# Performance work log

Measured on AMD Instinct MI355X. Metric: run time of the kernel, lower is better.

## Reference

```python
import jax, jax.numpy as jnp
import numpy as np

D_MODEL = 1024
HEAD_DIM = D_MODEL // 16  # num_heads=16, used only for the softmax scale
EPS = 1e-5


def _layernorm(x, g, b):
    mu = jnp.mean(x, axis=-1, keepdims=True)
    var = jnp.var(x, axis=-1, keepdims=True)
    return (x - mu) * jax.lax.rsqrt(var + EPS) * g + b


def setup_inputs() -> dict:
    key = jax.random.key(0)
    ks = jax.random.split(key, 16)
    d, dff = D_MODEL, 4 * D_MODEL
    s = 1.0 / np.sqrt(d)
    inp = {
        "x": jax.random.normal(ks[0], (4, 2048, d), dtype=jnp.float32),
        "wq": jax.random.normal(ks[1], (d, d), dtype=jnp.float32) * s,
        "bq": jnp.zeros((d,), jnp.float32),
        "wk": jax.random.normal(ks[2], (d, d), dtype=jnp.float32) * s,
        "bk": jnp.zeros((d,), jnp.float32),
        "wv": jax.random.normal(ks[3], (d, d), dtype=jnp.float32) * s,
        "bv": jnp.zeros((d,), jnp.float32),
        "wo": jax.random.normal(ks[4], (d, d), dtype=jnp.float32) * s,
        "bo": jnp.zeros((d,), jnp.float32),
        "w1": jax.random.normal(ks[5], (d, dff), dtype=jnp.float32) * s,
        "b1": jnp.zeros((dff,), jnp.float32),
        "w2": jax.random.normal(ks[6], (dff, d), dtype=jnp.float32) * (1.0 / np.sqrt(dff)),
        "b2": jnp.zeros((d,), jnp.float32),
        "g1": jnp.ones((d,), jnp.float32),
        "be1": jnp.zeros((d,), jnp.float32),
        "g2": jnp.ones((d,), jnp.float32),
        "be2": jnp.zeros((d,), jnp.float32),
    }
    return inp


def reference(x, wq, bq, wk, bk, wv, bv, wo, bo, w1, b1, w2, b2, g1, be1, g2, be2):
    # --- attention sub-block (NOTE: no head split in original module) ---
    residual = x
    h = _layernorm(x, g1, be1)
    q = h @ wq + bq
    k = h @ wk + bk
    v = h @ wv + bv
    scale = 1.0 / np.sqrt(HEAD_DIM)
    scores = jnp.einsum("bsd,btd->bst", q, k) * scale  # [B,S,S]
    attn = jax.nn.softmax(scores, axis=-1)
    ctx = jnp.einsum("bst,btd->bsd", attn, v)
    x = ctx @ wo + bo + residual
    # --- MLP sub-block ---
    residual = x
    h = _layernorm(x, g2, be2)
    h = jax.nn.gelu(h @ w1 + b1, approximate=False)
    return h @ w2 + b2 + residual
```

## Files before the change

kernel.cpp:

```cpp
#include <hip/hip_runtime.h>
#include <hip/hip_bf16.h>

typedef __hip_bfloat16 bf16;
typedef __attribute__((ext_vector_type(8))) short short8;
typedef __attribute__((ext_vector_type(4))) float floatx4;

__device__ __forceinline__ unsigned short f2bf(float x) {
  unsigned u = __builtin_bit_cast(unsigned, x);
  unsigned r = (u + 0x7fffu + ((u >> 16) & 1u)) >> 16;
  return (unsigned short)r;
}

#define GLL(g, l) __builtin_amdgcn_global_load_lds(                                  \
    (const __attribute__((address_space(1))) void*)(g),                              \
    (__attribute__((address_space(3))) void*)(l), 16, 0, 0)

template <int N> __device__ __forceinline__ void vmwait() {
  asm volatile("s_waitcnt vmcnt(%0)" ::"i"(N) : "memory");
}

__global__ __launch_bounds__(256) void wtrans_kernel(const float* __restrict__ in,
                                                     bf16* __restrict__ out,
                                                     int K, int N) {
  __shared__ float tile[32][33];
  int tx = threadIdx.x, ty = threadIdx.y;
  int n0 = blockIdx.x * 32, k0 = blockIdx.y * 32;
#pragma unroll
  for (int i = 0; i < 32; i += 8)
    tile[ty + i][tx] = in[(size_t)(k0 + ty + i) * N + (n0 + tx)];
  __syncthreads();
#pragma unroll
  for (int i = 0; i < 32; i += 8)
    out[(size_t)(n0 + ty + i) * K + (k0 + tx)] = __float2bfloat16(tile[tx][ty + i]);
}

__global__ __launch_bounds__(256) void ln_kernel(const float* __restrict__ x,
                                                 const float* __restrict__ g,
                                                 const float* __restrict__ b,
                                                 bf16* __restrict__ out) {
  const int D = 1024;
  size_t row = blockIdx.x;
  int t = threadIdx.x;
  float4 v = ((const float4*)(x + row * D))[t];
  float s  = v.x + v.y + v.z + v.w;
  float ss = v.x * v.x + v.y * v.y + v.z * v.z + v.w * v.w;
#pragma unroll
  for (int off = 32; off > 0; off >>= 1) {
    s  += __shfl_xor(s, off);
    ss += __shfl_xor(ss, off);
  }
  __shared__ float rs[4], rss[4];
  int wv = t >> 6;
  if ((t & 63) == 0) { rs[wv] = s; rss[wv] = ss; }
  __syncthreads();
  s  = rs[0] + rs[1] + rs[2] + rs[3];
  ss = rss[0] + rss[1] + rss[2] + rss[3];
  float mu  = s * (1.f / D);
  float inv = rsqrtf(ss * (1.f / D) - mu * mu + 1e-5f);
  float4 gv = ((const float4*)g)[t];
  float4 bv = ((const float4*)b)[t];
  ushort4 o;
  o.x = f2bf((v.x - mu) * inv * gv.x + bv.x);
  o.y = f2bf((v.y - mu) * inv * gv.y + bv.y);
  o.z = f2bf((v.z - mu) * inv * gv.z + bv.z);
  o.w = f2bf((v.w - mu) * inv * gv.w + bv.w);
  ((ushort4*)(out + row * D))[t] = o;
}

__global__ __launch_bounds__(256) void softmax_kernel(float* sc) {
  const int S = 2048;
  float* p = sc + (size_t)blockIdx.x * S;
  int t = threadIdx.x;
  float4 v0 = ((const float4*)p)[2 * t];
  float4 v1 = ((const float4*)p)[2 * t + 1];
  float f[8] = {v0.x, v0.y, v0.z, v0.w, v1.x, v1.y, v1.z, v1.w};
  float m = f[0];
#pragma unroll
  for (int j = 1; j < 8; ++j) m = fmaxf(m, f[j]);
#pragma unroll
  for (int off = 32; off > 0; off >>= 1) m = fmaxf(m, __shfl_xor(m, off));
  __shared__ float r1[4], r2[4];
  int wv = t >> 6;
  if ((t & 63) == 0) r1[wv] = m;
  __syncthreads();
  m = fmaxf(fmaxf(r1[0], r1[1]), fmaxf(r1[2], r1[3]));
  float s = 0.f;
#pragma unroll
  for (int j = 0; j < 8; ++j) { f[j] = __expf(f[j] - m); s += f[j]; }
#pragma unroll
  for (int off = 32; off > 0; off >>= 1) s += __shfl_xor(s, off);
  if ((t & 63) == 0) r2[wv] = s;
  __syncthreads();
  s = r2[0] + r2[1] + r2[2] + r2[3];
  float inv = 1.f / s;
  unsigned u0 = f2bf(f[0] * inv), u1 = f2bf(f[1] * inv);
  unsigned u2 = f2bf(f[2] * inv), u3 = f2bf(f[3] * inv);
  unsigned u4 = f2bf(f[4] * inv), u5 = f2bf(f[5] * inv);
  unsigned u6 = f2bf(f[6] * inv), u7 = f2bf(f[7] * inv);
  uint4 o;
  o.x = u0 | (u1 << 16);
  o.y = u2 | (u3 << 16);
  o.z = u4 | (u5 << 16);
  o.w = u6 | (u7 << 16);
  ((uint4*)p)[t] = o;
}

template <int NF, bool OUT_BF16, bool HAS_BIAS, bool HAS_RES, bool GELU, bool VTR>
__global__ __launch_bounds__(512, 2) void gemm4q(
    const bf16* __restrict__ A, int lda, size_t sA,
    const bf16* __restrict__ BT, int ldb, size_t sB,
    void* Cv, size_t sC,
    const float* __restrict__ bias, const float* res, bf16* vtr,
    int N, int K, float alpha, int gx, int gy) {
  constexpr int BN = NF * 64;
  constexpr int NI = NF / 2;
  constexpr int BHALF = NF == 4 ? 16384 : 8192;
  constexpr int W_A = 4;
  constexpr int W_B = NF == 4 ? 4 : 3;
  __shared__ __align__(16) char lds[65536 + (NF == 4 ? 65536 : 32768)];
  char* const ldsA = lds;
  char* const ldsB = lds + 65536;

  const int tid = threadIdx.x;
  const int lane = tid & 63;
  const int wave = tid >> 6;
  const int wm = wave >> 2, wn = wave & 3;
  const int lr = lane & 15, lq = lane >> 4;

  int id = blockIdx.x;
  const int nwg = gridDim.x;
  if ((nwg & 7) == 0) id = (id & 7) * (nwg >> 3) + (id >> 3);
  const int bx = id % gx;
  const int rem = id / gx;
  const int by = rem % gy;
  const int bz = rem / gy;
  const int m0 = by * 256, n0 = bx * BN;

  const int srow = tid >> 3;
  const int schunk = ((tid & 7) ^ (srow & 7)) * 8;
  const bf16* gA = A + sA * bz + (size_t)(m0 + srow) * lda + schunk;
  const bf16* gB = BT + sB * bz + (size_t)(n0 + srow) * ldb + schunk;

  const int nk = K >> 6;

  auto stA = [&](int tt, int h) {
    if (tt < nk) {
      const bf16* s = gA + (size_t)(h * 128) * lda + (size_t)tt * 64;
      char* d = ldsA + (((tt & 1) * 2 + h) << 14) + tid * 16;
      GLL(s, d);
      GLL(s + (size_t)64 * lda, d + 8192);
    }
  };
  auto stB = [&](int tt, int h) {
    if (tt < nk) {
      const bf16* s = gB + (size_t)(h * (BN / 2)) * ldb + (size_t)tt * 64;
      char* d = ldsB + ((tt & 1) * 2 + h) * BHALF + tid * 16;
      GLL(s, d);
      if constexpr (NF == 4) GLL(s + (size_t)64 * ldb, d + 8192);
    }
  };

  const int aB0 = (wm * 64 + lr) * 128 + ((lq ^ (lr & 7)) << 4);
  const int aB1 = aB0 ^ 64;
  const int bRow = (NF == 4) ? (wn * 32 + lr) : (wn * 16 + lr);
  const int bB0 = bRow * 128 + ((lq ^ (lr & 7)) << 4);
  const int bB1 = bB0 ^ 64;

  floatx4 acc[2][2][4][NI] = {};

  stA(0, 0); stB(0, 0); stB(0, 1); stA(0, 1);
  vmwait<W_B>();
  __builtin_amdgcn_s_barrier();

  for (int t = 0; t < nk; ++t) {
    const char* As0 = ldsA + (((t & 1) * 2 + 0) << 14);
    const char* As1 = ldsA + (((t & 1) * 2 + 1) << 14);
    const char* Bs0 = ldsB + ((t & 1) * 2 + 0) * BHALF;
    const char* Bs1 = ldsB + ((t & 1) * 2 + 1) * BHALF;
    short8 a0[4], a1[4], b0[NI], b1[NI];

#pragma unroll
    for (int mi = 0; mi < 4; ++mi) {
      a0[mi] = *(const short8*)(As0 + aB0 + mi * 2048);
      a1[mi] = *(const short8*)(As0 + aB1 + mi * 2048);
    }
#pragma unroll
    for (int ni = 0; ni < NI; ++ni) {
      b0[ni] = *(const short8*)(Bs0 + bB0 + ni * 2048);
      b1[ni] = *(const short8*)(Bs0 + bB1 + ni * 2048);
    }
    stA(t + 1, 0);
    asm volatile("s_waitcnt lgkmcnt(0)" ::: "memory");
    __builtin_amdgcn_sched_barrier(0);
    __builtin_amdgcn_s_setprio(1);
#pragma unroll
    for (int mi = 0; mi < 4; ++mi)
#pragma unroll
      for (int ni = 0; ni < NI; ++ni)
        acc[0][0][mi][ni] = __builtin_amdgcn_mfma_f32_16x16x32_bf16(a0[mi], b0[ni], acc[0][0][mi][ni], 0, 0, 0);
#pragma unroll
    for (int mi = 0; mi < 4; ++mi)
#pragma unroll
      for (int ni = 0; ni < NI; ++ni)
        acc[0][0][mi][ni] = __builtin_amdgcn_mfma_f32_16x16x32_bf16(a1[mi], b1[ni], acc[0][0][mi][ni], 0, 0, 0);
    __builtin_amdgcn_s_setprio(0);
    vmwait<W_A>();
    __builtin_amdgcn_s_barrier();

#pragma unroll
    for (int ni = 0; ni < NI; ++ni) {
      b0[ni] = *(const short8*)(Bs1 + bB0 + ni * 2048);
      b1[ni] = *(const short8*)(Bs1 + bB1 + ni * 2048);
    }
    stB(t + 1, 0);
    asm volatile("s_waitcnt lgkmcnt(0)" ::: "memory");
    __builtin_amdgcn_sched_barrier(0);
    __builtin_amdgcn_s_setprio(1);
#pragma unroll
    for (int mi = 0; mi < 4; ++mi)
#pragma unroll
      for (int ni = 0; ni < NI; ++ni)
        acc[0][1][mi][ni] = __builtin_amdgcn_mfma_f32_16x16x32_bf16(a0[mi], b0[ni], acc[0][1][mi][ni], 0, 0, 0);
#pragma unroll
    for (int mi = 0; mi < 4; ++mi)
#pragma unroll
      for (int ni = 0; ni < NI; ++ni)
        acc[0][1][mi][ni] = __builtin_amdgcn_mfma_f32_16x16x32_bf16(a1[mi], b1[ni], acc[0][1][mi][ni], 0, 0, 0);
    __builtin_amdgcn_s_setprio(0);
    vmwait<W_B>();
    __builtin_amdgcn_s_barrier();

#pragma unroll
    for (int mi = 0; mi < 4; ++mi) {
      a0[mi] = *(const short8*)(As1 + aB0 + mi * 2048);
      a1[mi] = *(const short8*)(As1 + aB1 + mi * 2048);
    }
    stB(t + 1, 1);
    asm volatile("s_waitcnt lgkmcnt(0)" ::: "memory");
    __builtin_amdgcn_sched_barrier(0);
    __builtin_amdgcn_s_setprio(1);
#pragma unroll
    for (int mi = 0; mi < 4; ++mi)
#pragma unroll
      for (int ni = 0; ni < NI; ++ni)
        acc[1][1][mi][ni] = __builtin_amdgcn_mfma_f32_16x16x32_bf16(a0[mi], b0[ni], acc[1][1][mi][ni], 0, 0, 0);
#pragma unroll
    for (int mi = 0; mi < 4; ++mi)
#pragma unroll
      for (int ni = 0; ni < NI; ++ni)
        acc[1][1][mi][ni] = __builtin_amdgcn_mfma_f32_16x16x32_bf16(a1[mi], b1[ni], acc[1][1][mi][ni], 0, 0, 0);
    __builtin_amdgcn_s_setprio(0);
    __builtin_amdgcn_s_barrier();

#pragma unroll
    for (int ni = 0; ni < NI; ++ni) {
      b0[ni] = *(const short8*)(Bs0 + bB0 + ni * 2048);
      b1[ni] = *(const short8*)(Bs0 + bB1 + ni * 2048);
    }
    stA(t + 1, 1);
    asm volatile("s_waitcnt lgkmcnt(0)" ::: "memory");
    __builtin_amdgcn_sched_barrier(0);
    __builtin_amdgcn_s_setprio(1);
#pragma unroll
    for (int mi = 0; mi < 4; ++mi)
#pragma unroll
      for (int ni = 0; ni < NI; ++ni)
        acc[1][0][mi][ni] = __builtin_amdgcn_mfma_f32_16x16x32_bf16(a0[mi], b0[ni], acc[1][0][mi][ni], 0, 0, 0);
#pragma unroll
    for (int mi = 0; mi < 4; ++mi)
#pragma unroll
      for (int ni = 0; ni < NI; ++ni)
        acc[1][0][mi][ni] = __builtin_amdgcn_mfma_f32_16x16x32_bf16(a1[mi], b1[ni], acc[1][0][mi][ni], 0, 0, 0);
    __builtin_amdgcn_s_setprio(0);
    vmwait<W_B>();
    __builtin_amdgcn_s_barrier();
  }

  float* Cf = (float*)Cv;
  bf16* Cb = (bf16*)Cv;
  const size_t cb = sC * bz;
#pragma unroll
  for (int mq = 0; mq < 2; ++mq)
#pragma unroll
    for (int nq = 0; nq < 2; ++nq)
#pragma unroll
      for (int mi = 0; mi < 4; ++mi) {
        const int row = m0 + mq * 128 + wm * 64 + mi * 16 + lq * 4;
#pragma unroll
        for (int ni = 0; ni < NI; ++ni) {
          const int col = n0 + nq * (BN / 2) + wn * (BN / 8) + ni * 16 + lr;
          const float bb = HAS_BIAS ? bias[col] : 0.f;
#pragma unroll
          for (int r = 0; r < 4; ++r) {
            float val = acc[mq][nq][mi][ni][r] * alpha + bb;
            if (GELU) val = 0.5f * val * (1.f + erff(val * 0.70710678118654752f));
            if (HAS_RES) val += res[(size_t)(row + r) * N + col];
            const size_t idx = cb + (size_t)(row + r) * N + col;
            if (OUT_BF16) Cb[idx] = __float2bfloat16(val);
            else Cf[idx] = val;
            if (VTR) {
              if (col >= 2048) {
                const int rr = row + r;
                vtr[(((size_t)(rr >> 11) << 10) + (col - 2048)) * 2048 + (rr & 2047)] =
                    __float2bfloat16(val);
              }
            }
          }
        }
      }
}

extern "C" void kernel_launch(void* const* d_in, const int* in_sizes, int n_in,
                              void* d_out, int out_size, void* d_ws, size_t ws_size,
                              hipStream_t stream) {
  const int B = 4, S = 2048, D = 1024, DFF = 4096;
  const int M = B * S;
  const float* x   = (const float*)d_in[0];
  const float* wq  = (const float*)d_in[1];
  const float* bq  = (const float*)d_in[2];
  const float* wk  = (const float*)d_in[3];
  const float* bk  = (const float*)d_in[4];
  const float* wv  = (const float*)d_in[5];
  const float* bv  = (const float*)d_in[6];
  const float* wo  = (const float*)d_in[7];
  const float* bo  = (const float*)d_in[8];
  const float* w1  = (const float*)d_in[9];
  const float* b1  = (const float*)d_in[10];
  const float* w2  = (const float*)d_in[11];
  const float* b2  = (const float*)d_in[12];
  const float* g1  = (const float*)d_in[13];
  const float* be1 = (const float*)d_in[14];
  const float* g2  = (const float*)d_in[15];
  const float* be2 = (const float*)d_in[16];
  float* out = (float*)d_out;

  char* wsb = (char*)d_ws;
  const size_t MB1 = 1ull << 20;
  bf16* wqkvT = (bf16*)(wsb + 0 * MB1);
  bf16* woT   = (bf16*)(wsb + 6 * MB1);
  bf16* w1T   = (bf16*)(wsb + 8 * MB1);
  bf16* w2T   = (bf16*)(wsb + 16 * MB1);
  float* bqkv = (float*)(wsb + 24 * MB1);
  bf16* h     = (bf16*)(wsb + 25 * MB1);
  bf16* qkv   = (bf16*)(wsb + 41 * MB1);
  bf16* hidden = (bf16*)(wsb + 41 * MB1);
  bf16* vTall = (bf16*)(wsb + 89 * MB1);
  float* sc   = (float*)(wsb + 105 * MB1);

  int chunk = 1;
  if (ws_size > 105 * MB1) {
    size_t c = (ws_size - 105 * MB1) / (16 * MB1);
    chunk = (int)(c > 4 ? 4 : (c < 1 ? 1 : c));
  }

  dim3 tb(32, 8);
  wtrans_kernel<<<dim3(32, 32), tb, 0, stream>>>(wq, wqkvT, D, D);
  wtrans_kernel<<<dim3(32, 32), tb, 0, stream>>>(wk, wqkvT + (size_t)1024 * 1024, D, D);
  wtrans_kernel<<<dim3(32, 32), tb, 0, stream>>>(wv, wqkvT + (size_t)2048 * 1024, D, D);
  wtrans_kernel<<<dim3(32, 32), tb, 0, stream>>>(wo, woT, D, D);
  wtrans_kernel<<<dim3(128, 32), tb, 0, stream>>>(w1, w1T, D, DFF);
  wtrans_kernel<<<dim3(32, 128), tb, 0, stream>>>(w2, w2T, DFF, D);
  hipMemcpyAsync(bqkv, bq, 4096, hipMemcpyDeviceToDevice, stream);
  hipMemcpyAsync(bqkv + 1024, bk, 4096, hipMemcpyDeviceToDevice, stream);
  hipMemcpyAsync(bqkv + 2048, bv, 4096, hipMemcpyDeviceToDevice, stream);

  ln_kernel<<<M, 256, 0, stream>>>(x, g1, be1, h);

  gemm4q<2, true, true, false, false, true><<<24 * 32, 512, 0, stream>>>(
      h, D, 0, wqkvT, D, 0, qkv, 0, bqkv, nullptr, vTall, 3072, D, 1.f, 24, 32);

  for (int b0 = 0; b0 < B; b0 += chunk) {
    int c = (B - b0 < chunk) ? (B - b0) : chunk;
    gemm4q<4, false, false, false, false, false><<<64 * c, 512, 0, stream>>>(
        qkv + (size_t)b0 * S * 3072, 3072, (size_t)S * 3072,
        qkv + (size_t)b0 * S * 3072 + 1024, 3072, (size_t)S * 3072,
        sc, (size_t)S * S, nullptr, nullptr, nullptr, S, D, 0.125f, 8, 8);
    softmax_kernel<<<c * S, 256, 0, stream>>>(sc);
    gemm4q<2, true, false, false, false, false><<<64 * c, 512, 0, stream>>>(
        (const bf16*)sc, 2 * S, (size_t)S * 2 * S,
        vTall + (size_t)b0 * D * S, S, (size_t)D * S,
        h + (size_t)b0 * S * D, (size_t)S * D, nullptr, nullptr, nullptr, D, S, 1.f, 8, 8);
  }

  gemm4q<2, false, true, true, false, false><<<8 * 32, 512, 0, stream>>>(
      h, D, 0, woT, D, 0, out, 0, bo, x, nullptr, D, D, 1.f, 8, 32);

  ln_kernel<<<M, 256, 0, stream>>>(out, g2, be2, h);

  gemm4q<4, true, true, false, true, false><<<16 * 32, 512, 0, stream>>>(
      h, D, 0, w1T, D, 0, hidden, 0, b1, nullptr, nullptr, DFF, D, 1.f, 16, 32);

  gemm4q<2, false, true, true, false, false><<<8 * 32, 512, 0, stream>>>(
      hidden, DFF, 0, w2T, DFF, 0, out, 0, b2, out, nullptr, D, DFF, 1.f, 8, 32);
}
```

Baseline: 473.4 us.

## Peel last K-iteration and use inline ds_read with immediate offsets in GEMM

Rewrites the GEMM main loop to peel the final K tile into an epilogue. This removes the per-load bounds checks on the global-to-LDS prefetch, and the peeled tile drains outstanding loads with exact vmcnt waits. LDS fragment reads become inline-asm ds_read_b128 with immediate offsets from a 32-bit LDS base, which cuts address arithmetic. The fourth quarter-step now reuses A fragments from the third step, with B in separate registers and one fewer barrier per iteration. The hand-counted waitcnt values and the larger code size add risk of ordering bugs or register pressure.

```diff
diff --git a/kernel.cpp b/kernel.cpp
--- a/kernel.cpp
+++ b/kernel.cpp
@@ -4,6 +4,7 @@
 typedef __hip_bfloat16 bf16;
 typedef __attribute__((ext_vector_type(8))) short short8;
 typedef __attribute__((ext_vector_type(4))) float floatx4;
+typedef __attribute__((address_space(3))) char c3;
 
 __device__ __forceinline__ unsigned short f2bf(float x) {
   unsigned u = __builtin_bit_cast(unsigned, x);
@@ -17,6 +18,15 @@
 
 template <int N> __device__ __forceinline__ void vmwait() {
   asm volatile("s_waitcnt vmcnt(%0)" ::"i"(N) : "memory");
+}
+template <int OFF> __device__ __forceinline__ short8 dsr(unsigned a) {
+  short8 r;
+  asm volatile("ds_read_b128 %0, %1 offset:%2" : "=v"(r) : "v"(a), "i"(OFF));
+  return r;
+}
+__device__ __forceinline__ void lgkm0_fence() {
+  asm volatile("s_waitcnt lgkmcnt(0)" ::: "memory");
+  __builtin_amdgcn_sched_barrier(0);
 }
 
 __global__ __launch_bounds__(256) void wtrans_kernel(const float* __restrict__ in,
@@ -106,7 +116,7 @@
 }
 
 template <int NF, bool OUT_BF16, bool HAS_BIAS, bool HAS_RES, bool GELU, bool VTR>
-__global__ __launch_bounds__(512, 2) void gemm4q(
+__global__ __launch_bounds__(512, 2) void gemm6(
     const bf16* __restrict__ A, int lda, size_t sA,
     const bf16* __restrict__ BT, int ldb, size_t sB,
     void* Cv, size_t sC,
@@ -115,11 +125,11 @@
   constexpr int BN = NF * 64;
   constexpr int NI = NF / 2;
   constexpr int BHALF = NF == 4 ? 16384 : 8192;
-  constexpr int W_A = 4;
-  constexpr int W_B = NF == 4 ? 4 : 3;
-  __shared__ __align__(16) char lds[65536 + (NF == 4 ? 65536 : 32768)];
-  char* const ldsA = lds;
-  char* const ldsB = lds + 65536;
+  constexpr int LB = NF == 4 ? 2 : 1;
+  constexpr int W_AB = 2 + LB;
+  __shared__ __align__(16) char lds_storage[65536 + (NF == 4 ? 65536 : 32768)];
+  const unsigned ldsAu = (unsigned)(uintptr_t)(c3*)lds_storage;
+  const unsigned ldsBu = ldsAu + 65536;
 
   const int tid = threadIdx.x;
   const int lane = tid & 63;
@@ -144,54 +154,45 @@
   const int nk = K >> 6;
 
   auto stA = [&](int tt, int h) {
-    if (tt < nk) {
-      const bf16* s = gA + (size_t)(h * 128) * lda + (size_t)tt * 64;
-      char* d = ldsA + (((tt & 1) * 2 + h) << 14) + tid * 16;
-      GLL(s, d);
-      GLL(s + (size_t)64 * lda, d + 8192);
-    }
+    const bf16* s = gA + (size_t)(h * 128) * lda + (size_t)tt * 64;
+    char* d = lds_storage + (((tt & 1) * 2 + h) << 14) + tid * 16;
+    GLL(s, d);
+    GLL(s + (size_t)64 * lda, d + 8192);
   };
   auto stB = [&](int tt, int h) {
-    if (tt < nk) {
-      const bf16* s = gB + (size_t)(h * (BN / 2)) * ldb + (size_t)tt * 64;
-      char* d = ldsB + ((tt & 1) * 2 + h) * BHALF + tid * 16;
-      GLL(s, d);
-      if constexpr (NF == 4) GLL(s + (size_t)64 * ldb, d + 8192);
-    }
+    const bf16* s = gB + (size_t)(h * (BN / 2)) * ldb + (size_t)tt * 64;
+    char* d = lds_storage + 65536 + ((tt & 1) * 2 + h) * BHALF + tid * 16;
+    GLL(s, d);
+    if constexpr (NF == 4) GLL(s + (size_t)64 * ldb, d + 8192);
   };
 
-  const int aB0 = (wm * 64 + lr) * 128 + ((lq ^ (lr & 7)) << 4);
-  const int aB1 = aB0 ^ 64;
-  const int bRow = (NF == 4) ? (wn * 32 + lr) : (wn * 16 + lr);
-  const int bB0 = bRow * 128 + ((lq ^ (lr & 7)) << 4);
-  const int bB1 = bB0 ^ 64;
+  const unsigned aB0 = (wm * 64 + lr) * 128 + ((lq ^ (lr & 7)) << 4);
+  const unsigned bRow = (NF == 4) ? (wn * 32 + lr) : (wn * 16 + lr);
+  const unsigned bB0 = bRow * 128 + ((lq ^ (lr & 7)) << 4);
 
   floatx4 acc[2][2][4][NI] = {};
 
   stA(0, 0); stB(0, 0); stB(0, 1); stA(0, 1);
-  vmwait<W_B>();
+  vmwait<W_AB>();
   __builtin_amdgcn_s_barrier();
 
-  for (int t = 0; t < nk; ++t) {
-    const char* As0 = ldsA + (((t & 1) * 2 + 0) << 14);
-    const char* As1 = ldsA + (((t & 1) * 2 + 1) << 14);
-    const char* Bs0 = ldsB + ((t & 1) * 2 + 0) * BHALF;
-    const char* Bs1 = ldsB + ((t & 1) * 2 + 1) * BHALF;
-    short8 a0[4], a1[4], b0[NI], b1[NI];
-
-#pragma unroll
-    for (int mi = 0; mi < 4; ++mi) {
-      a0[mi] = *(const short8*)(As0 + aB0 + mi * 2048);
-      a1[mi] = *(const short8*)(As0 + aB1 + mi * 2048);
-    }
-#pragma unroll
-    for (int ni = 0; ni < NI; ++ni) {
-      b0[ni] = *(const short8*)(Bs0 + bB0 + ni * 2048);
-      b1[ni] = *(const short8*)(Bs0 + bB1 + ni * 2048);
-    }
+  for (int t = 0; t + 1 < nk; ++t) {
+    const unsigned As0 = ldsAu + (((t & 1) * 2 + 0) << 14);
+    const unsigned As1 = As0 + 16384;
+    const unsigned Bs0 = ldsBu + ((t & 1) * 2 + 0) * BHALF;
+    const unsigned Bs1 = Bs0 + BHALF;
+    short8 a0[4], a1[4], b0[NI], b1[NI], c0[NI], c1[NI];
+
     stA(t + 1, 0);
-    asm volatile("s_waitcnt lgkmcnt(0)" ::: "memory");
-    __builtin_amdgcn_sched_barrier(0);
+    {
+      const unsigned aA = As0 + aB0, aX = aA ^ 64;
+      a0[0] = dsr<0>(aA);  a0[1] = dsr<2048>(aA);  a0[2] = dsr<4096>(aA);  a0[3] = dsr<6144>(aA);
+      a1[0] = dsr<0>(aX);  a1[1] = dsr<2048>(aX);  a1[2] = dsr<4096>(aX);  a1[3] = dsr<6144>(aX);
+      const unsigned bA = Bs0 + bB0, bX = bA ^ 64;
+      b0[0] = dsr<0>(bA); b1[0] = dsr<0>(bX);
+      if constexpr (NI > 1) { b0[1] = dsr<2048>(bA); b1[1] = dsr<2048>(bX); }
+    }
+    lgkm0_fence();
     __builtin_amdgcn_s_setprio(1);
 #pragma unroll
     for (int mi = 0; mi < 4; ++mi)
@@ -204,17 +205,16 @@
       for (int ni = 0; ni < NI; ++ni)
         acc[0][0][mi][ni] = __builtin_amdgcn_mfma_f32_16x16x32_bf16(a1[mi], b1[ni], acc[0][0][mi][ni], 0, 0, 0);
     __builtin_amdgcn_s_setprio(0);
-    vmwait<W_A>();
+    vmwait<4>();
     __builtin_amdgcn_s_barrier();
 
-#pragma unroll
-    for (int ni = 0; ni < NI; ++ni) {
-      b0[ni] = *(const short8*)(Bs1 + bB0 + ni * 2048);
-      b1[ni] = *(const short8*)(Bs1 + bB1 + ni * 2048);
-    }
     stB(t + 1, 0);
-    asm volatile("s_waitcnt lgkmcnt(0)" ::: "memory");
-    __builtin_amdgcn_sched_barrier(0);
+    {
+      const unsigned bA = Bs1 + bB0, bX = bA ^ 64;
+      b0[0] = dsr<0>(bA); b1[0] = dsr<0>(bX);
+      if constexpr (NI > 1) { b0[1] = dsr<2048>(bA); b1[1] = dsr<2048>(bX); }
+    }
+    lgkm0_fence();
     __builtin_amdgcn_s_setprio(1);
 #pragma unroll
     for (int mi = 0; mi < 4; ++mi)
@@ -227,17 +227,16 @@
       for (int ni = 0; ni < NI; ++ni)
         acc[0][1][mi][ni] = __builtin_amdgcn_mfma_f32_16x16x32_bf16(a1[mi], b1[ni], acc[0][1][mi][ni], 0, 0, 0);
     __builtin_amdgcn_s_setprio(0);
-    vmwait<W_B>();
+    vmwait<W_AB>();
     __builtin_amdgcn_s_barrier();
 
-#pragma unroll
-    for (int mi = 0; mi < 4; ++mi) {
-      a0[mi] = *(const short8*)(As1 + aB0 + mi * 2048);
-      a1[mi] = *(const short8*)(As1 + aB1 + mi * 2048);
-    }
     stB(t + 1, 1);
-    asm volatile("s_waitcnt lgkmcnt(0)" ::: "memory");
-    __builtin_amdgcn_sched_barrier(0);
+    {
+      const unsigned aA = As1 + aB0, aX = aA ^ 64;
+      a0[0] = dsr<0>(aA);  a0[1] = dsr<2048>(aA);  a0[2] = dsr<4096>(aA);  a0[3] = dsr<6144>(aA);
+      a1[0] = dsr<0>(aX);  a1[1] = dsr<2048>(aX);  a1[2] = dsr<4096>(aX);  a1[3] = dsr<6144>(aX);
+    }
+    lgkm0_fence();
     __builtin_amdgcn_s_setprio(1);
 #pragma unroll
     for (int mi = 0; mi < 4; ++mi)
@@ -250,30 +249,110 @@
       for (int ni = 0; ni < NI; ++ni)
         acc[1][1][mi][ni] = __builtin_amdgcn_mfma_f32_16x16x32_bf16(a1[mi], b1[ni], acc[1][1][mi][ni], 0, 0, 0);
     __builtin_amdgcn_s_setprio(0);
+    stA(t + 1, 1);
+    {
+      const unsigned bA = Bs0 + bB0, bX = bA ^ 64;
+      c0[0] = dsr<0>(bA); c1[0] = dsr<0>(bX);
+      if constexpr (NI > 1) { c0[1] = dsr<2048>(bA); c1[1] = dsr<2048>(bX); }
+    }
+    lgkm0_fence();
+    __builtin_amdgcn_s_setprio(1);
+#pragma unroll
+    for (int mi = 0; mi < 4; ++mi)
+#pragma unroll
+      for (int ni = 0; ni < NI; ++ni)
+        acc[1][0][mi][ni] = __builtin_amdgcn_mfma_f32_16x16x32_bf16(a0[mi], c0[ni], acc[1][0][mi][ni], 0, 0, 0);
+#pragma unroll
+    for (int mi = 0; mi < 4; ++mi)
+#pragma unroll
+      for (int ni = 0; ni < NI; ++ni)
+        acc[1][0][mi][ni] = __builtin_amdgcn_mfma_f32_16x16x32_bf16(a1[mi], c1[ni], acc[1][0][mi][ni], 0, 0, 0);
+    __builtin_amdgcn_s_setprio(0);
+    vmwait<W_AB>();
     __builtin_amdgcn_s_barrier();
-
-#pragma unroll
-    for (int ni = 0; ni < NI; ++ni) {
-      b0[ni] = *(const short8*)(Bs0 + bB0 + ni * 2048);
-      b1[ni] = *(const short8*)(Bs0 + bB1 + ni * 2048);
-    }
-    stA(t + 1, 1);
-    asm volatile("s_waitcnt lgkmcnt(0)" ::: "memory");
-    __builtin_amdgcn_sched_barrier(0);
-    __builtin_amdgcn_s_setprio(1);
-#pragma unroll
-    for (int mi = 0; mi < 4; ++mi)
-#pragma unroll
-      for (int ni = 0; ni < NI; ++ni)
-        acc[1][0][mi][ni] = __builtin_amdgcn_mfma_f32_16x16x32_bf16(a0[mi], b0[ni], acc[1][0][mi][ni], 0, 0, 0);
-#pragma unroll
-    for (int mi = 0; mi < 4; ++mi)
-#pragma unroll
-      for (int ni = 0; ni < NI; ++ni)
-        acc[1][0][mi][ni] = __builtin_amdgcn_mfma_f32_16x16x32_bf16(a1[mi], b1[ni], acc[1][0][mi][ni], 0, 0, 0);
-    __builtin_amdgcn_s_setprio(0);
-    vmwait<W_B>();
+  }
+
+  {
+    const int t = nk - 1;
+    const unsigned As0 = ldsAu + (((t & 1) * 2 + 0) << 14);
+    const unsigned As1 = As0 + 16384;
+    const unsigned Bs0 = ldsBu + ((t & 1) * 2 + 0) * BHALF;
+    const unsigned Bs1 = Bs0 + BHALF;
+    short8 a0[4], a1[4], b0[NI], b1[NI], c0[NI], c1[NI];
+
+    {
+      const unsigned aA = As0 + aB0, aX = aA ^ 64;
+      a0[0] = dsr<0>(aA);  a0[1] = dsr<2048>(aA);  a0[2] = dsr<4096>(aA);  a0[3] = dsr<6144>(aA);
+      a1[0] = dsr<0>(aX);  a1[1] = dsr<2048>(aX);  a1[2] = dsr<4096>(aX);  a1[3] = dsr<6144>(aX);
+      const unsigned bA = Bs0 + bB0, bX = bA ^ 64;
+      b0[0] = dsr<0>(bA); b1[0] = dsr<0>(bX);
+      if constexpr (NI > 1) { b0[1] = dsr<2048>(bA); b1[1] = dsr<2048>(bX); }
+    }
+    lgkm0_fence();
+#pragma unroll
+    for (int mi = 0; mi < 4; ++mi)
+#pragma unroll
+      for (int ni = 0; ni < NI; ++ni)
+        acc[0][0][mi][ni] = __builtin_amdgcn_mfma_f32_16x16x32_bf16(a0[mi], b0[ni], acc[0][0][mi][ni], 0, 0, 0);
+#pragma unroll
+    for (int mi = 0; mi < 4; ++mi)
+#pragma unroll
+      for (int ni = 0; ni < NI; ++ni)
+        acc[0][0][mi][ni] = __builtin_amdgcn_mfma_f32_16x16x32_bf16(a1[mi], b1[ni], acc[0][0][mi][ni], 0, 0, 0);
+    vmwait<2>();
     __builtin_amdgcn_s_barrier();
+
+    {
+      const unsigned bA = Bs1 + bB0, bX = bA ^ 64;
+      b0[0] = dsr<0>(bA); b1[0] = dsr<0>(bX);
+      if constexpr (NI > 1) { b0[1] = dsr<2048>(bA); b1[1] = dsr<2048>(bX); }
+    }
+    lgkm0_fence();
+#pragma unroll
+    for (int mi = 0; mi < 4; ++mi)
+#pragma unroll
+      for (int ni = 0; ni < NI; ++ni)
+        acc[0][1][mi][ni] = __builtin_amdgcn_mfma_f32_16x16x32_bf16(a0[mi], b0[ni], acc[0][1][mi][ni], 0, 0, 0);
+#pragma unroll
+    for (int mi = 0; mi < 4; ++mi)
+#pragma unroll
+      for (int ni = 0; ni < NI; ++ni)
+        acc[0][1][mi][ni] = __builtin_amdgcn_mfma_f32_16x16x32_bf16(a1[mi], b1[ni], acc[0][1][mi][ni], 0, 0, 0);
+    vmwait<0>();
+    __builtin_amdgcn_s_barrier();
+
+    {
+      const unsigned aA = As1 + aB0, aX = aA ^ 64;
+      a0[0] = dsr<0>(aA);  a0[1] = dsr<2048>(aA);  a0[2] = dsr<4096>(aA);  a0[3] = dsr<6144>(aA);
+      a1[0] = dsr<0>(aX);  a1[1] = dsr<2048>(aX);  a1[2] = dsr<4096>(aX);  a1[3] = dsr<6144>(aX);
+    }
+    lgkm0_fence();
+#pragma unroll
+    for (int mi = 0; mi < 4; ++mi)
+#pragma unroll
+      for (int ni = 0; ni < NI; ++ni)
+        acc[1][1][mi][ni] = __builtin_amdgcn_mfma_f32_16x16x32_bf16(a0[mi], b0[ni], acc[1][1][mi][ni], 0, 0, 0);
+#pragma unroll
+    for (int mi = 0; mi < 4; ++mi)
+#pragma unroll
+      for (int ni = 0; ni < NI; ++ni)
+        acc[1][1][mi][ni] = __builtin_amdgcn_mfma_f32_16x16x32_bf16(a1[mi], b1[ni], acc[1][1][mi][ni], 0, 0, 0);
+    {
+      const unsigned bA = Bs0 + bB0, bX = bA ^ 64;
+      c0[0] = dsr<0>(bA); c1[0] = dsr<0>(bX);
+      if constexpr (NI > 1) { c0[1] = dsr<2048>(bA); c1[1] = dsr<2048>(bX); }
+    }
+    lgkm0_fence();
+#pragma unroll
+    for (int mi = 0; mi < 4; ++mi)
+#pragma unroll
+      for (int ni = 0; ni < NI; ++ni)
+        acc[1][0][mi][ni] = __builtin_amdgcn_mfma_f32_16x16x32_bf16(a0[mi], c0[ni], acc[1][0][mi][ni], 0, 0, 0);
+#pragma unroll
+    for (int mi = 0; mi < 4; ++mi)
+#pragma unroll
+      for (int ni = 0; ni < NI; ++ni)
+        acc[1][0][mi][ni] = __builtin_amdgcn_mfma_f32_16x16x32_bf16(a1[mi], c1[ni], acc[1][0][mi][ni], 0, 0, 0);
   }
 
   float* Cf = (float*)Cv;
@@ -366,30 +445,30 @@
 
   ln_kernel<<<M, 256, 0, stream>>>(x, g1, be1, h);
 
-  gemm4q<2, true, true, false, false, true><<<24 * 32, 512, 0, stream>>>(
+  gemm6<2, true, true, false, false, true><<<24 * 32, 512, 0, stream>>>(
       h, D, 0, wqkvT, D, 0, qkv, 0, bqkv, nullptr, vTall, 3072, D, 1.f, 24, 32);
 
   for (int b0 = 0; b0 < B; b0 += chunk) {
     int c = (B - b0 < chunk) ? (B - b0) : chunk;
-    gemm4q<4, false, false, false, false, false><<<64 * c, 512, 0, stream>>>(
+    gemm6<4, false, false, false, false, false><<<64 * c, 512, 0, stream>>>(
         qkv + (size_t)b0 * S * 3072, 3072, (size_t)S * 3072,
         qkv + (size_t)b0 * S * 3072 + 1024, 3072, (size_t)S * 3072,
         sc, (size_t)S * S, nullptr, nullptr, nullptr, S, D, 0.125f, 8, 8);
     softmax_kernel<<<c * S, 256, 0, stream>>>(sc);
-    gemm4q<2, true, false, false, false, false><<<64 * c, 512, 0, stream>>>(
+    gemm6<2, true, false, false, false, false><<<64 * c, 512, 0, stream>>>(
         (const bf16*)sc, 2 * S, (size_t)S * 2 * S,
         vTall + (size_t)b0 * D * S, S, (size_t)D * S,
         h + (size_t)b0 * S * D, (size_t)S * D, nullptr, nullptr, nullptr, D, S, 1.f, 8, 8);
   }
 
-  gemm4q<2, false, true, true, false, false><<<8 * 32, 512, 0, stream>>>(
+  gemm6<2, false, true, true, false, false><<<8 * 32, 512, 0, stream>>>(
       h, D, 0, woT, D, 0, out, 0, bo, x, nullptr, D, D, 1.f, 8, 32);
 
   ln_kernel<<<M, 256, 0, stream>>>(out, g2, be2, h);
 
-  gemm4q<4, true, true, false, true, false><<<16 * 32, 512, 0, stream>>>(
+  gemm6<4, true, true, false, true, false><<<16 * 32, 512, 0, stream>>>(
       h, D, 0, w1T, D, 0, hidden, 0, b1, nullptr, nullptr, DFF, D, 1.f, 16, 32);
 
-  gemm4q<2, false, true, true, false, false><<<8 * 32, 512, 0, stream>>>(
+  gemm6<2, false, true, true, false, false><<<8 * 32, 512, 0, stream>>>(
       hidden, DFF, 0, w2T, DFF, 0, out, 0, b2, out, nullptr, D, DFF, 1.f, 8, 32);
 }
```

Measured after the change: 464.2 us. No clear change (-1.9%).

## Deepen GEMM global-to-LDS prefetch to two tiles and reuse B fragments

Applied to the files above, without the earlier changes.

The GEMM main loop is restructured so global→LDS loads are issued two K-tiles ahead instead of one, with peeled final iterations that drop the bounds checks and use tuned vmcnt waits. The first B-half fragments are kept in registers and reused for the last quadrant, which removes one LDS read phase and one barrier per tile. LDS reads go through inline ds_read_b128 with immediate offsets to cut address arithmetic. In exchange, register pressure rises from the extra fragment buffers, and the hand-set wait counts must be exactly right for correctness.

```diff
diff --git a/kernel.cpp b/kernel.cpp
--- a/kernel.cpp
+++ b/kernel.cpp
@@ -4,6 +4,9 @@
 typedef __hip_bfloat16 bf16;
 typedef __attribute__((ext_vector_type(8))) short short8;
 typedef __attribute__((ext_vector_type(4))) float floatx4;
+typedef __attribute__((address_space(3))) char c3;
+
+template <int V> struct ic { static constexpr int value = V; };
 
 __device__ __forceinline__ unsigned short f2bf(float x) {
   unsigned u = __builtin_bit_cast(unsigned, x);
@@ -17,6 +20,15 @@
 
 template <int N> __device__ __forceinline__ void vmwait() {
   asm volatile("s_waitcnt vmcnt(%0)" ::"i"(N) : "memory");
+}
+template <int OFF> __device__ __forceinline__ short8 dsr(unsigned a) {
+  short8 r;
+  asm volatile("ds_read_b128 %0, %1 offset:%2" : "=v"(r) : "v"(a), "i"(OFF));
+  return r;
+}
+__device__ __forceinline__ void lgkm0_fence() {
+  asm volatile("s_waitcnt lgkmcnt(0)" ::: "memory");
+  __builtin_amdgcn_sched_barrier(0);
 }
 
 __global__ __launch_bounds__(256) void wtrans_kernel(const float* __restrict__ in,
@@ -106,7 +118,7 @@
 }
 
 template <int NF, bool OUT_BF16, bool HAS_BIAS, bool HAS_RES, bool GELU, bool VTR>
-__global__ __launch_bounds__(512, 2) void gemm4q(
+__global__ __launch_bounds__(512, 2) void gemm7(
     const bf16* __restrict__ A, int lda, size_t sA,
     const bf16* __restrict__ BT, int ldb, size_t sB,
     void* Cv, size_t sC,
@@ -115,11 +127,9 @@
   constexpr int BN = NF * 64;
   constexpr int NI = NF / 2;
   constexpr int BHALF = NF == 4 ? 16384 : 8192;
-  constexpr int W_A = 4;
-  constexpr int W_B = NF == 4 ? 4 : 3;
-  __shared__ __align__(16) char lds[65536 + (NF == 4 ? 65536 : 32768)];
-  char* const ldsA = lds;
-  char* const ldsB = lds + 65536;
+  __shared__ __align__(16) char lds_storage[65536 + (NF == 4 ? 65536 : 32768)];
+  const unsigned ldsAu = (unsigned)(uintptr_t)(c3*)lds_storage;
+  const unsigned ldsBu = ldsAu + 65536;
 
   const int tid = threadIdx.x;
   const int lane = tid & 63;
@@ -144,137 +154,127 @@
   const int nk = K >> 6;
 
   auto stA = [&](int tt, int h) {
-    if (tt < nk) {
-      const bf16* s = gA + (size_t)(h * 128) * lda + (size_t)tt * 64;
-      char* d = ldsA + (((tt & 1) * 2 + h) << 14) + tid * 16;
-      GLL(s, d);
-      GLL(s + (size_t)64 * lda, d + 8192);
+    const bf16* s = gA + (size_t)(h * 128) * lda + (size_t)tt * 64;
+    char* d = lds_storage + (((tt & 1) * 2 + h) << 14) + tid * 16;
+    GLL(s, d);
+    GLL(s + (size_t)64 * lda, d + 8192);
+  };
+  auto stB = [&](int tt, int h) {
+    const bf16* s = gB + (size_t)(h * (BN / 2)) * ldb + (size_t)tt * 64;
+    char* d = lds_storage + 65536 + ((tt & 1) * 2 + h) * BHALF + tid * 16;
+    GLL(s, d);
+    if constexpr (NF == 4) GLL(s + (size_t)64 * ldb, d + 8192);
+  };
+
+  const unsigned aB0 = (wm * 64 + lr) * 128 + ((lq ^ (lr & 7)) << 4);
+  const unsigned bRow = (NF == 4) ? (wn * 32 + lr) : (wn * 16 + lr);
+  const unsigned bB0 = bRow * 128 + ((lq ^ (lr & 7)) << 4);
+
+  floatx4 acc[2][2][4][NI] = {};
+
+  stA(0, 0); stB(0, 0); stB(0, 1); stA(0, 1);
+  stA(1, 0); stB(1, 0); stB(1, 1);
+  vmwait<NF == 4 ? 10 : 7>();
+  __builtin_amdgcn_s_barrier();
+
+  auto tile_body = [&](int t, auto modeC) {
+    constexpr int MODE = decltype(modeC)::value;
+    constexpr int W0  = MODE < 2 ? (NF == 4 ? 10 : 8) : 2;
+    constexpr int W1  = MODE == 0 ? (NF == 4 ? 12 : 9)
+                                  : (MODE == 1 ? (NF == 4 ? 8 : 6) : 0);
+    constexpr int W23 = MODE == 0 ? (NF == 4 ? 10 : 7)
+                                  : (MODE == 1 ? (NF == 4 ? 4 : 3) : -1);
+    const unsigned As0 = ldsAu + (((t & 1) * 2 + 0) << 14);
+    const unsigned As1 = As0 + 16384;
+    const unsigned Bs0 = ldsBu + ((t & 1) * 2 + 0) * BHALF;
+    const unsigned Bs1 = Bs0 + BHALF;
+    short8 a0[4], a1[4], b0[NI], b1[NI], bb0[NI], bb1[NI];
+
+    {
+      const unsigned aA = As0 + aB0, aX = aA ^ 64;
+      a0[0] = dsr<0>(aA);  a0[1] = dsr<2048>(aA);  a0[2] = dsr<4096>(aA);  a0[3] = dsr<6144>(aA);
+      a1[0] = dsr<0>(aX);  a1[1] = dsr<2048>(aX);  a1[2] = dsr<4096>(aX);  a1[3] = dsr<6144>(aX);
+      const unsigned bA = Bs0 + bB0, bX = bA ^ 64;
+      bb0[0] = dsr<0>(bA); bb1[0] = dsr<0>(bX);
+      if constexpr (NI > 1) { bb0[1] = dsr<2048>(bA); bb1[1] = dsr<2048>(bX); }
+    }
+    if constexpr (MODE < 2) stA(t + 1, 1);
+    lgkm0_fence();
+    __builtin_amdgcn_s_setprio(1);
+#pragma unroll
+    for (int mi = 0; mi < 4; ++mi)
+#pragma unroll
+      for (int ni = 0; ni < NI; ++ni)
+        acc[0][0][mi][ni] = __builtin_amdgcn_mfma_f32_16x16x32_bf16(a0[mi], bb0[ni], acc[0][0][mi][ni], 0, 0, 0);
+#pragma unroll
+    for (int mi = 0; mi < 4; ++mi)
+#pragma unroll
+      for (int ni = 0; ni < NI; ++ni)
+        acc[0][0][mi][ni] = __builtin_amdgcn_mfma_f32_16x16x32_bf16(a1[mi], bb1[ni], acc[0][0][mi][ni], 0, 0, 0);
+    __builtin_amdgcn_s_setprio(0);
+    vmwait<W0>();
+    __builtin_amdgcn_s_barrier();
+
+    {
+      const unsigned bA = Bs1 + bB0, bX = bA ^ 64;
+      b0[0] = dsr<0>(bA); b1[0] = dsr<0>(bX);
+      if constexpr (NI > 1) { b0[1] = dsr<2048>(bA); b1[1] = dsr<2048>(bX); }
+    }
+    if constexpr (MODE == 0) { stA(t + 2, 0); stB(t + 2, 0); }
+    lgkm0_fence();
+    __builtin_amdgcn_s_setprio(1);
+#pragma unroll
+    for (int mi = 0; mi < 4; ++mi)
+#pragma unroll
+      for (int ni = 0; ni < NI; ++ni)
+        acc[0][1][mi][ni] = __builtin_amdgcn_mfma_f32_16x16x32_bf16(a0[mi], b0[ni], acc[0][1][mi][ni], 0, 0, 0);
+#pragma unroll
+    for (int mi = 0; mi < 4; ++mi)
+#pragma unroll
+      for (int ni = 0; ni < NI; ++ni)
+        acc[0][1][mi][ni] = __builtin_amdgcn_mfma_f32_16x16x32_bf16(a1[mi], b1[ni], acc[0][1][mi][ni], 0, 0, 0);
+    __builtin_amdgcn_s_setprio(0);
+    vmwait<W1>();
+    __builtin_amdgcn_s_barrier();
+
+    {
+      const unsigned aA = As1 + aB0, aX = aA ^ 64;
+      a0[0] = dsr<0>(aA);  a0[1] = dsr<2048>(aA);  a0[2] = dsr<4096>(aA);  a0[3] = dsr<6144>(aA);
+      a1[0] = dsr<0>(aX);  a1[1] = dsr<2048>(aX);  a1[2] = dsr<4096>(aX);  a1[3] = dsr<6144>(aX);
+    }
+    if constexpr (MODE == 0) stB(t + 2, 1);
+    lgkm0_fence();
+    __builtin_amdgcn_s_setprio(1);
+#pragma unroll
+    for (int mi = 0; mi < 4; ++mi)
+#pragma unroll
+      for (int ni = 0; ni < NI; ++ni)
+        acc[1][1][mi][ni] = __builtin_amdgcn_mfma_f32_16x16x32_bf16(a0[mi], b0[ni], acc[1][1][mi][ni], 0, 0, 0);
+#pragma unroll
+    for (int mi = 0; mi < 4; ++mi)
+#pragma unroll
+      for (int ni = 0; ni < NI; ++ni)
+        acc[1][1][mi][ni] = __builtin_amdgcn_mfma_f32_16x16x32_bf16(a1[mi], b1[ni], acc[1][1][mi][ni], 0, 0, 0);
+#pragma unroll
+    for (int mi = 0; mi < 4; ++mi)
+#pragma unroll
+      for (int ni = 0; ni < NI; ++ni)
+        acc[1][0][mi][ni] = __builtin_amdgcn_mfma_f32_16x16x32_bf16(a0[mi], bb0[ni], acc[1][0][mi][ni], 0, 0, 0);
+#pragma unroll
+    for (int mi = 0; mi < 4; ++mi)
+#pragma unroll
+      for (int ni = 0; ni < NI; ++ni)
+        acc[1][0][mi][ni] = __builtin_amdgcn_mfma_f32_16x16x32_bf16(a1[mi], bb1[ni], acc[1][0][mi][ni], 0, 0, 0);
+    __builtin_amdgcn_s_setprio(0);
+    if constexpr (W23 >= 0) {
+      vmwait<W23>();
+      __builtin_amdgcn_s_barrier();
     }
   };
-  auto stB = [&](int tt, int h) {
-    if (tt < nk) {
-      const bf16* s = gB + (size_t)(h * (BN / 2)) * ldb + (size_t)tt * 64;
-      char* d = ldsB + ((tt & 1) * 2 + h) * BHALF + tid * 16;
-      GLL(s, d);
-      if constexpr (NF == 4) GLL(s + (size_t)64 * ldb, d + 8192);
-    }
-  };
-
-  const int aB0 = (wm * 64 + lr) * 128 + ((lq ^ (lr & 7)) << 4);
-  const int aB1 = aB0 ^ 64;
-  const int bRow = (NF == 4) ? (wn * 32 + lr) : (wn * 16 + lr);
-  const int bB0 = bRow * 128 + ((lq ^ (lr & 7)) << 4);
-  const int bB1 = bB0 ^ 64;
-
-  floatx4 acc[2][2][4][NI] = {};
-
-  stA(0, 0); stB(0, 0); stB(0, 1); stA(0, 1);
-  vmwait<W_B>();
-  __builtin_amdgcn_s_barrier();
-
-  for (int t = 0; t < nk; ++t) {
-    const char* As0 = ldsA + (((t & 1) * 2 + 0) << 14);
-    const char* As1 = ldsA + (((t & 1) * 2 + 1) << 14);
-    const char* Bs0 = ldsB + ((t & 1) * 2 + 0) * BHALF;
-    const char* Bs1 = ldsB + ((t & 1) * 2 + 1) * BHALF;
-    short8 a0[4], a1[4], b0[NI], b1[NI];
-
-#pragma unroll
-    for (int mi = 0; mi < 4; ++mi) {
-      a0[mi] = *(const short8*)(As0 + aB0 + mi * 2048);
-      a1[mi] = *(const short8*)(As0 + aB1 + mi * 2048);
-    }
-#pragma unroll
-    for (int ni = 0; ni < NI; ++ni) {
-      b0[ni] = *(const short8*)(Bs0 + bB0 + ni * 2048);
-      b1[ni] = *(const short8*)(Bs0 + bB1 + ni * 2048);
-    }
-    stA(t + 1, 0);
-    asm volatile("s_waitcnt lgkmcnt(0)" ::: "memory");
-    __builtin_amdgcn_sched_barrier(0);
-    __builtin_amdgcn_s_setprio(1);
-#pragma unroll
-    for (int mi = 0; mi < 4; ++mi)
-#pragma unroll
-      for (int ni = 0; ni < NI; ++ni)
-        acc[0][0][mi][ni] = __builtin_amdgcn_mfma_f32_16x16x32_bf16(a0[mi], b0[ni], acc[0][0][mi][ni], 0, 0, 0);
-#pragma unroll
-    for (int mi = 0; mi < 4; ++mi)
-#pragma unroll
-      for (int ni = 0; ni < NI; ++ni)
-        acc[0][0][mi][ni] = __builtin_amdgcn_mfma_f32_16x16x32_bf16(a1[mi], b1[ni], acc[0][0][mi][ni], 0, 0, 0);
-    __builtin_amdgcn_s_setprio(0);
-    vmwait<W_A>();
-    __builtin_amdgcn_s_barrier();
-
-#pragma unroll
-    for (int ni = 0; ni < NI; ++ni) {
-      b0[ni] = *(const short8*)(Bs1 + bB0 + ni * 2048);
-      b1[ni] = *(const short8*)(Bs1 + bB1 + ni * 2048);
-    }
-    stB(t + 1, 0);
-    asm volatile("s_waitcnt lgkmcnt(0)" ::: "memory");
-    __builtin_amdgcn_sched_barrier(0);
-    __builtin_amdgcn_s_setprio(1);
-#pragma unroll
-    for (int mi = 0; mi < 4; ++mi)
-#pragma unroll
-      for (int ni = 0; ni < NI; ++ni)
-        acc[0][1][mi][ni] = __builtin_amdgcn_mfma_f32_16x16x32_bf16(a0[mi], b0[ni], acc[0][1][mi][ni], 0, 0, 0);
-#pragma unroll
-    for (int mi = 0; mi < 4; ++mi)
-#pragma unroll
-      for (int ni = 0; ni < NI; ++ni)
-        acc[0][1][mi][ni] = __builtin_amdgcn_mfma_f32_16x16x32_bf16(a1[mi], b1[ni], acc[0][1][mi][ni], 0, 0, 0);
-    __builtin_amdgcn_s_setprio(0);
-    vmwait<W_B>();
-    __builtin_amdgcn_s_barrier();
-
-#pragma unroll
-    for (int mi = 0; mi < 4; ++mi) {
-      a0[mi] = *(const short8*)(As1 + aB0 + mi * 2048);
-      a1[mi] = *(const short8*)(As1 + aB1 + mi * 2048);
-    }
-    stB(t + 1, 1);
-    asm volatile("s_waitcnt lgkmcnt(0)" ::: "memory");
-    __builtin_amdgcn_sched_barrier(0);
-    __builtin_amdgcn_s_setprio(1);
-#pragma unroll
-    for (int mi = 0; mi < 4; ++mi)
-#pragma unroll
-      for (int ni = 0; ni < NI; ++ni)
-        acc[1][1][mi][ni] = __builtin_amdgcn_mfma_f32_16x16x32_bf16(a0[mi], b0[ni], acc[1][1][mi][ni], 0, 0, 0);
-#pragma unroll
-    for (int mi = 0; mi < 4; ++mi)
-#pragma unroll
-      for (int ni = 0; ni < NI; ++ni)
-        acc[1][1][mi][ni] = __builtin_amdgcn_mfma_f32_16x16x32_bf16(a1[mi], b1[ni], acc[1][1][mi][ni], 0, 0, 0);
-    __builtin_amdgcn_s_setprio(0);
-    __builtin_amdgcn_s_barrier();
-
-#pragma unroll
-    for (int ni = 0; ni < NI; ++ni) {
-      b0[ni] = *(const short8*)(Bs0 + bB0 + ni * 2048);
-      b1[ni] = *(const short8*)(Bs0 + bB1 + ni * 2048);
-    }
-    stA(t + 1, 1);
-    asm volatile("s_waitcnt lgkmcnt(0)" ::: "memory");
-    __builtin_amdgcn_sched_barrier(0);
-    __builtin_amdgcn_s_setprio(1);
-#pragma unroll
-    for (int mi = 0; mi < 4; ++mi)
-#pragma unroll
-      for (int ni = 0; ni < NI; ++ni)
-        acc[1][0][mi][ni] = __builtin_amdgcn_mfma_f32_16x16x32_bf16(a0[mi], b0[ni], acc[1][0][mi][ni], 0, 0, 0);
-#pragma unroll
-    for (int mi = 0; mi < 4; ++mi)
-#pragma unroll
-      for (int ni = 0; ni < NI; ++ni)
-        acc[1][0][mi][ni] = __builtin_amdgcn_mfma_f32_16x16x32_bf16(a1[mi], b1[ni], acc[1][0][mi][ni], 0, 0, 0);
-    __builtin_amdgcn_s_setprio(0);
-    vmwait<W_B>();
-    __builtin_amdgcn_s_barrier();
-  }
+
+  for (int t = 0; t + 2 < nk; ++t) tile_body(t, ic<0>{});
+  tile_body(nk - 2, ic<1>{});
+  tile_body(nk - 1, ic<2>{});
 
   float* Cf = (float*)Cv;
   bf16* Cb = (bf16*)Cv;
@@ -366,30 +366,30 @@
 
   ln_kernel<<<M, 256, 0, stream>>>(x, g1, be1, h);
 
-  gemm4q<2, true, true, false, false, true><<<24 * 32, 512, 0, stream>>>(
+  gemm7<2, true, true, false, false, true><<<24 * 32, 512, 0, stream>>>(
       h, D, 0, wqkvT, D, 0, qkv, 0, bqkv, nullptr, vTall, 3072, D, 1.f, 24, 32);
 
   for (int b0 = 0; b0 < B; b0 += chunk) {
     int c = (B - b0 < chunk) ? (B - b0) : chunk;
-    gemm4q<4, false, false, false, false, false><<<64 * c, 512, 0, stream>>>(
+    gemm7<4, false, false, false, false, false><<<64 * c, 512, 0, stream>>>(
         qkv + (size_t)b0 * S * 3072, 3072, (size_t)S * 3072,
         qkv + (size_t)b0 * S * 3072 + 1024, 3072, (size_t)S * 3072,
         sc, (size_t)S * S, nullptr, nullptr, nullptr, S, D, 0.125f, 8, 8);
     softmax_kernel<<<c * S, 256, 0, stream>>>(sc);
-    gemm4q<2, true, false, false, false, false><<<64 * c, 512, 0, stream>>>(
+    gemm7<2, true, false, false, false, false><<<64 * c, 512, 0, stream>>>(
         (const bf16*)sc, 2 * S, (size_t)S * 2 * S,
         vTall + (size_t)b0 * D * S, S, (size_t)D * S,
         h + (size_t)b0 * S * D, (size_t)S * D, nullptr, nullptr, nullptr, D, S, 1.f, 8, 8);
   }
 
-  gemm4q<2, false, true, true, false, false><<<8 * 32, 512, 0, stream>>>(
+  gemm7<2, false, true, true, false, false><<<8 * 32, 512, 0, stream>>>(
       h, D, 0, woT, D, 0, out, 0, bo, x, nullptr, D, D, 1.f, 8, 32);
 
   ln_kernel<<<M, 256, 0, stream>>>(out, g2, be2, h);
 
-  gemm4q<4, true, true, false, true, false><<<16 * 32, 512, 0, stream>>>(
+  gemm7<4, true, true, false, true, false><<<16 * 32, 512, 0, stream>>>(
       h, D, 0, w1T, D, 0, hidden, 0, b1, nullptr, nullptr, DFF, D, 1.f, 16, 32);
 
-  gemm4q<2, false, true, true, false, false><<<8 * 32, 512, 0, stream>>>(
+  gemm7<2, false, true, true, false, false><<<8 * 32, 512, 0, stream>>>(
       hidden, DFF, 0, w2T, DFF, 0, out, 0, b2, out, nullptr, D, DFF, 1.f, 8, 32);
 }
```

Result: faster. 459.2 us (-3.0%).
